# Optimization experiments

Hardware: AMD Instinct MI355X
Metric: run time of the kernel (lower is better)

## Reference

```python
import jax, jax.numpy as jnp
import numpy as np
import math

NUM_BUCKETS = 32
MAX_DISTANCE = 128


def _relative_position_buckets(seq_len):
    # bidirectional T5-style buckets, matching the torch reference exactly
    pos = jnp.arange(seq_len)
    rp = pos[None, :] - pos[:, None]                # [S, S]
    nb = NUM_BUCKETS // 2                            # bidirectional halving
    buckets = (rp > 0).astype(jnp.int32) * nb
    rp = jnp.abs(rp)
    max_exact = nb // 2
    is_small = rp < max_exact
    rp_f = jnp.maximum(rp, 1).astype(jnp.float32)    # avoid log(0); masked by is_small
    rp_large = max_exact + (
        jnp.log(rp_f / max_exact) / math.log(MAX_DISTANCE / max_exact) * (nb - max_exact)
    ).astype(jnp.int32)                              # trunc toward zero, like .to(torch.long)
    rp_large = jnp.minimum(rp_large, nb - 1)
    return buckets + jnp.where(is_small, rp, rp_large)  # [S, S] int32 in [0, 31]


def setup_inputs() -> dict:
    key = jax.random.key(0)
    kq, kk, kv, km, kb = jax.random.split(key, 5)
    B, H, S, D = 4, 4, 2048, 64
    return {
        "query": jax.random.normal(kq, (B, H, S, D), dtype=jnp.float32),
        "key": jax.random.normal(kk, (B, H, S, D), dtype=jnp.float32),
        "value": jax.random.normal(kv, (B, H, S, D), dtype=jnp.float32),
        "mask": jax.random.randint(km, (B, 1, 1, S), 0, 2, dtype=jnp.int32),
        "bias_table": jax.random.normal(kb, (512, 4), dtype=jnp.float32) * 0.02,
    }


def reference(query, key, value, mask, bias_table):
    B, H, S, D = query.shape
    attn = jnp.einsum("bhqd,bhkd->bhqk", query, key)          # [B,H,S,S]
    rel = _relative_position_buckets(S)                        # [S,S]
    bias = bias_table[rel]                                     # [S,S,H]
    bias = jnp.transpose(bias, (2, 0, 1))[None]                # [1,H,S,S]
    scores = (attn + bias) / math.sqrt(D)                      # bias added pre-scale, as in torch
    scores = jnp.where(mask == 0, jnp.float32(-1e9), scores)
    p_attn = jax.nn.softmax(scores, axis=-1)
    out = jnp.einsum("bhqk,bhkd->bhqd", p_attn, value)
    return out, p_attn
```

## Files before the change

kernel.cpp:

```cpp
#include <hip/hip_runtime.h>
#include <math.h>

typedef __attribute__((ext_vector_type(8))) short short8;
typedef __attribute__((ext_vector_type(4))) float f32x4;
typedef _Float16 f16x8 __attribute__((ext_vector_type(8)));
typedef _Float16 f16x4v __attribute__((ext_vector_type(4)));
typedef unsigned short u16;

#define S_LEN 2048
#define D_HEAD 64
#define C2 0.18033688011112043f

static __device__ __forceinline__ float exp2v(float x) {
    float r; asm("v_exp_f32 %0, %1" : "=v"(r) : "v"(x)); return r;
}

static __device__ __forceinline__ void gl_lds16(const void* g, void* l) {
    __builtin_amdgcn_global_load_lds(
        (const __attribute__((address_space(1))) unsigned int*)g,
        (__attribute__((address_space(3))) unsigned int*)l, 16, 0, 0);
}

__global__ void prep_bias(const float* __restrict__ table, float* __restrict__ bias_d) {
    int idx = blockIdx.x * blockDim.x + threadIdx.x;
    if (idx >= 4096) return;
    int delta = idx - 2047;
    int bpos = (delta > 0) ? 16 : 0;
    int ad = delta < 0 ? -delta : delta;
    int rel;
    if (ad < 8) {
        rel = bpos + ad;
    } else {
        float rp = (float)ad;
        int lg = 8 + (int)(logf(rp / 8.0f) / 2.772588722239781f * 8.0f);
        if (lg > 15) lg = 15;
        rel = bpos + lg;
    }
    #pragma unroll
    for (int h = 0; h < 4; ++h)
        bias_d[h * 4096 + idx] = C2 * table[rel * 4 + h];
}

__global__ void prep_half(const float* __restrict__ src, _Float16* __restrict__ dst) {
    size_t i8 = ((size_t)blockIdx.x * 256 + threadIdx.x) * 8;
    f32x4 a = *(const f32x4*)(src + i8);
    f32x4 b = *(const f32x4*)(src + i8 + 4);
    f16x8 h;
    h[0] = (_Float16)a[0]; h[1] = (_Float16)a[1];
    h[2] = (_Float16)a[2]; h[3] = (_Float16)a[3];
    h[4] = (_Float16)b[0]; h[5] = (_Float16)b[1];
    h[6] = (_Float16)b[2]; h[7] = (_Float16)b[3];
    *(f16x8*)(dst + i8) = h;
}

__global__ void prep_vt(const float* __restrict__ V, _Float16* __restrict__ vt) {
    __shared__ float tile[64][65];
    const int bh = blockIdx.y;
    const int k0 = blockIdx.x * 64;
    const int t = threadIdx.x;
    {
        int r = t >> 2, c0 = (t & 3) * 16;
        const float* src = V + ((size_t)bh * S_LEN + k0 + r) * D_HEAD + c0;
        #pragma unroll
        for (int i = 0; i < 16; i += 4) {
            f32x4 v = *(const f32x4*)(src + i);
            tile[r][c0 + i + 0] = v[0];
            tile[r][c0 + i + 1] = v[1];
            tile[r][c0 + i + 2] = v[2];
            tile[r][c0 + i + 3] = v[3];
        }
    }
    __syncthreads();
    {
        int d = t >> 2, kc = (t & 3) * 16;
        size_t ob = ((size_t)bh * D_HEAD + d) * S_LEN + k0 + kc;
        #pragma unroll
        for (int half = 0; half < 2; ++half) {
            f16x8 hv;
            #pragma unroll
            for (int i = 0; i < 8; ++i)
                hv[i] = (_Float16)tile[kc + half * 8 + i][d];
            *(f16x8*)(vt + ob + half * 8) = hv;
        }
    }
}

__launch_bounds__(512, 6)
__global__ void attn_main(const float* __restrict__ Q, const int* __restrict__ mask,
                          const float* __restrict__ bias2,
                          const _Float16* __restrict__ kh_g,
                          const _Float16* __restrict__ vt_g,
                          float* __restrict__ outp, float* __restrict__ p_out) {
    __shared__ __align__(16) char smem[50688];
    _Float16* pbuf = (_Float16*)(smem + 32768);
    float* stats = (float*)(smem + 50176);

    const int tid = threadIdx.x;
    const int w = tid >> 6, l = tid & 63;
    const int wq = w & 3, wk = w >> 2;
    const int g = l >> 4, lq = l & 15;
    const int r7 = lq & 7;
    const int bid = blockIdx.x;
    const int bh = bid & 15, b = bh >> 2, h = bh & 3;
    const int q0 = (bid >> 4) * 64;

    const float* Qp = Q + (size_t)bh * (S_LEN * D_HEAD);
    const int* mp = mask + b * S_LEN;
    const _Float16* khp = kh_g + (size_t)bh * (S_LEN * D_HEAD);
    const _Float16* vhp = vt_g + (size_t)bh * (S_LEN * D_HEAD);

    _Float16* qarea = (_Float16*)smem;
    {
        int sr = tid >> 3, tb = tid & 7;
        const float* src = Qp + (size_t)(q0 + sr) * D_HEAD + tb * 8;
        f32x4 a = *(const f32x4*)src;
        f32x4 c = *(const f32x4*)(src + 4);
        f16x8 hv;
        hv[0] = (_Float16)a[0]; hv[1] = (_Float16)a[1];
        hv[2] = (_Float16)a[2]; hv[3] = (_Float16)a[3];
        hv[4] = (_Float16)c[0]; hv[5] = (_Float16)c[1];
        hv[6] = (_Float16)c[2]; hv[7] = (_Float16)c[3];
        *(f16x8*)(qarea + sr * 64 + ((tb ^ (sr & 7)) * 8)) = hv;
    }
    __syncthreads();
    f16x8 qf[2];
    const int qrow = 16 * wq + lq;
    #pragma unroll
    for (int c = 0; c < 2; ++c)
        qf[c] = *(const f16x8*)(qarea + qrow * 64 + ((4 * c + g) ^ r7) * 8);
    __syncthreads();

    const int qq = q0 + qrow;

    const int rr3 = tid >> 3;
    const int ub0 = (((tid & 7) ^ (rr3 & 7)) * 8);
    const _Float16* s1a = khp + (size_t)rr3 * 64 + ub0;
    gl_lds16(s1a, smem + tid * 16);
    gl_lds16(s1a + 4096, smem + 8192 + tid * 16);
    __syncthreads();

    const int* mP1 = mp + 64 * wk + 4 * g;
    const float* bP1 = bias2 + h * 4096 + 2047 - qq + 64 * wk + 4 * g;
    float lsum = 0.0f;
    for (int t = 0; t < 16; ++t) {
        const char* kb = smem + (t & 1) * 16384;
        int4 mv[4]; float bv[4][4];
        #pragma unroll
        for (int t2 = 0; t2 < 4; ++t2) {
            mv[t2] = *(const int4*)(mP1 + 16 * t2);
            #pragma unroll
            for (int j = 0; j < 4; ++j) bv[t2][j] = bP1[16 * t2 + j];
        }
        if (t < 15) {
            s1a += 8192;
            char* nb = smem + ((t + 1) & 1) * 16384 + tid * 16;
            gl_lds16(s1a, nb);
            gl_lds16(s1a + 4096, nb + 8192);
        }
        __builtin_amdgcn_sched_barrier(0);
        #pragma unroll
        for (int t2 = 0; t2 < 4; ++t2) {
            const int krow = 64 * wk + 16 * t2 + lq;
            f32x4 acc = {0.f, 0.f, 0.f, 0.f};
            #pragma unroll
            for (int c = 0; c < 2; ++c) {
                f16x8 af = *(const f16x8*)(kb + krow * 128 + ((4 * c + g) ^ r7) * 16);
                acc = __builtin_amdgcn_mfma_f32_16x16x32_f16(af, qf[c], acc, 0, 0, 0);
            }
            float s0 = mv[t2].x ? fmaf(acc[0], C2, bv[t2][0]) : -1e9f;
            float s1 = mv[t2].y ? fmaf(acc[1], C2, bv[t2][1]) : -1e9f;
            float s2 = mv[t2].z ? fmaf(acc[2], C2, bv[t2][2]) : -1e9f;
            float s3 = mv[t2].w ? fmaf(acc[3], C2, bv[t2][3]) : -1e9f;
            lsum += exp2v(s0) + exp2v(s1) + exp2v(s2) + exp2v(s3);
        }
        mP1 += 128; bP1 += 128;
        asm volatile("s_waitcnt vmcnt(0)" ::: "memory");
        __builtin_amdgcn_sched_barrier(0);
        __builtin_amdgcn_s_barrier();
        __builtin_amdgcn_sched_barrier(0);
    }
    lsum += __shfl_xor(lsum, 16);
    lsum += __shfl_xor(lsum, 32);
    if (g == 0) stats[wk * 64 + qrow] = lsum;

    const _Float16* sKh = khp + (size_t)rr3 * 64 + ub0;
    const _Float16* sVh = vhp + (size_t)rr3 * 2048 + ub0;
    gl_lds16(sKh, smem + tid * 16);
    gl_lds16(sVh, smem + 8192 + tid * 16);
    __syncthreads();
    float lr2q;
    {
        float L = stats[qrow] + stats[64 + qrow];
        float lg; asm("v_log_f32 %0, %1" : "=v"(lg) : "v"(L));
        lr2q = -lg;
    }

    f32x4 acco[4] = {{0.f,0.f,0.f,0.f},{0.f,0.f,0.f,0.f},{0.f,0.f,0.f,0.f},{0.f,0.f,0.f,0.f}};
    const int* mP = mp + 32 * wk + 4 * g;
    const float* bP = bias2 + h * 4096 + 2047 - qq + 32 * wk + 4 * g;
    const int kAoff0 = (32 * wk + lq) * 128;
    const int voffb = lq * 128 + ((4 * wk + g) ^ r7) * 16;
    _Float16* pwr = pbuf + qrow * 136 + 32 * wk + 4 * g;
    const _Float16* prd = pbuf + qrow * 136 + 32 * wk + 8 * g;
    const int frow = 16 * (w >> 1) + (l >> 4);
    const int fcol = 64 * (w & 1) + (l & 15) * 4;
    const _Float16* frd = pbuf + frow * 136 + fcol;
    float* pF = p_out + (size_t)bh * (S_LEN * S_LEN)
              + (size_t)(q0 + frow) * S_LEN + fcol;

    for (int t = 0; t < 32; ++t) {
        const int cb = (t & 1) * 16384;
        const int pt = (t & 1) * 64;
        int4 mv[2]; float bv[2][4];
        #pragma unroll
        for (int t2 = 0; t2 < 2; ++t2) {
            mv[t2] = *(const int4*)(mP + 16 * t2);
            #pragma unroll
            for (int j = 0; j < 4; ++j) bv[t2][j] = bP[16 * t2 + j];
        }
        if (t < 31) {
            sKh += 4096; sVh += 64;
            char* d0 = smem + ((t + 1) & 1) * 16384 + tid * 16;
            gl_lds16(sKh, d0);
            gl_lds16(sVh, d0 + 8192);
        }
        __builtin_amdgcn_sched_barrier(0);
        #pragma unroll
        for (int t2 = 0; t2 < 2; ++t2) {
            const char* kbase = smem + cb + kAoff0 + t2 * 2048;
            f32x4 acc = {0.f, 0.f, 0.f, 0.f};
            #pragma unroll
            for (int c = 0; c < 2; ++c) {
                f16x8 ah = *(const f16x8*)(kbase + ((4 * c + g) ^ r7) * 16);
                acc = __builtin_amdgcn_mfma_f32_16x16x32_f16(ah, qf[c], acc, 0, 0, 0);
            }
            float p0 = exp2v(mv[t2].x ? fmaf(acc[0], C2, bv[t2][0]) + lr2q : -1e9f);
            float p1 = exp2v(mv[t2].y ? fmaf(acc[1], C2, bv[t2][1]) + lr2q : -1e9f);
            float p2 = exp2v(mv[t2].z ? fmaf(acc[2], C2, bv[t2][2]) + lr2q : -1e9f);
            float p3 = exp2v(mv[t2].w ? fmaf(acc[3], C2, bv[t2][3]) + lr2q : -1e9f);
            f16x4v ph4;
            ph4[0] = (_Float16)p0; ph4[1] = (_Float16)p1;
            ph4[2] = (_Float16)p2; ph4[3] = (_Float16)p3;
            *(f16x4v*)(pwr + pt + 16 * t2) = ph4;
        }
        const f16x8 pf = *(const f16x8*)(prd + pt);
        #pragma unroll
        for (int n = 0; n < 4; ++n) {
            const f16x8 bhf = *(const f16x8*)(smem + cb + 8192 + voffb + n * 2048);
            acco[n] = __builtin_amdgcn_mfma_f32_16x16x32_f16(pf, bhf, acco[n], 0, 0, 0);
        }
        mP += 64; bP += 64;
        if (t & 1) {
            asm volatile("s_waitcnt lgkmcnt(0)" ::: "memory");
            __builtin_amdgcn_sched_barrier(0);
            __builtin_amdgcn_s_barrier();
            __builtin_amdgcn_sched_barrier(0);
            #pragma unroll
            for (int i = 0; i < 4; ++i) {
                f16x4v v = *(const f16x4v*)(frd + i * (4 * 136));
                f32x4 wv;
                wv[0] = (float)v[0]; wv[1] = (float)v[1];
                wv[2] = (float)v[2]; wv[3] = (float)v[3];
                *(f32x4*)(pF + (size_t)(4 * i) * S_LEN) = wv;
            }
            pF += 128;
            __builtin_amdgcn_sched_barrier(0);
            asm volatile("s_waitcnt vmcnt(4)" ::: "memory");
        } else {
            asm volatile("s_waitcnt vmcnt(0)" ::: "memory");
        }
        __builtin_amdgcn_sched_barrier(0);
        __builtin_amdgcn_s_barrier();
        __builtin_amdgcn_sched_barrier(0);
    }

    float* ored = (float*)smem;
    __syncthreads();
    if (wk == 1) {
        #pragma unroll
        for (int n = 0; n < 4; ++n)
            #pragma unroll
            for (int r = 0; r < 4; ++r)
                ored[(wq * 16 + 4 * g + r) * 64 + 16 * n + lq] = acco[n][r];
    }
    __syncthreads();
    if (wk == 0) {
        #pragma unroll
        for (int n = 0; n < 4; ++n) {
            #pragma unroll
            for (int r = 0; r < 4; ++r) {
                float v = acco[n][r] + ored[(wq * 16 + 4 * g + r) * 64 + 16 * n + lq];
                outp[((size_t)bh * S_LEN + q0 + 16 * wq + 4 * g + r) * D_HEAD + 16 * n + lq] = v;
            }
        }
    }
}

extern "C" void kernel_launch(void* const* d_in, const int* in_sizes, int n_in,
                              void* d_out, int out_size, void* d_ws, size_t ws_size,
                              hipStream_t stream) {
    const float* Q = (const float*)d_in[0];
    const float* K = (const float*)d_in[1];
    const float* V = (const float*)d_in[2];
    const int* mask = (const int*)d_in[3];
    const float* table = (const float*)d_in[4];

    float* outp = (float*)d_out;
    float* p_out = outp + (size_t)4 * 4 * 2048 * 64;

    float* bias_d = (float*)d_ws;
    _Float16* kh = (_Float16*)((char*)d_ws + 65536);
    _Float16* vt = kh + (size_t)16 * S_LEN * D_HEAD;

    prep_bias<<<16, 256, 0, stream>>>(table, bias_d);
    prep_half<<<1024, 256, 0, stream>>>(K, kh);
    prep_vt<<<dim3(32, 16), 256, 0, stream>>>(V, vt);
    attn_main<<<512, 512, 0, stream>>>(Q, mask, bias_d, kh, vt, outp, p_out);
}
```

Measured before the change: 104.5 us.

## Switch attention kernel to 4 waves each owning full key range per query block

The main kernel drops from 8 waves (split across query and key halves) to 4 waves, each owning 16 query rows across all keys. This removes the cross-wave LDS reduction of row sums and output accumulators, and gives each wave a private P buffer so the probability stream-out needs no extra block barrier. Mask and bias are premerged, with the log-sum added before the loop. Each thread now issues more MFMAs and global-to-LDS loads per tile, and there are fewer waves per block to hide latency.

```diff
diff --git a/kernel.cpp b/kernel.cpp
--- a/kernel.cpp
+++ b/kernel.cpp
@@ -1,11 +1,9 @@
 #include <hip/hip_runtime.h>
 #include <math.h>
 
-typedef __attribute__((ext_vector_type(8))) short short8;
 typedef __attribute__((ext_vector_type(4))) float f32x4;
 typedef _Float16 f16x8 __attribute__((ext_vector_type(8)));
 typedef _Float16 f16x4v __attribute__((ext_vector_type(4)));
-typedef unsigned short u16;
 
 #define S_LEN 2048
 #define D_HEAD 64
@@ -85,19 +83,16 @@
     }
 }
 
-__launch_bounds__(512, 6)
+__launch_bounds__(256, 3)
 __global__ void attn_main(const float* __restrict__ Q, const int* __restrict__ mask,
                           const float* __restrict__ bias2,
                           const _Float16* __restrict__ kh_g,
                           const _Float16* __restrict__ vt_g,
                           float* __restrict__ outp, float* __restrict__ p_out) {
-    __shared__ __align__(16) char smem[50688];
-    _Float16* pbuf = (_Float16*)(smem + 32768);
-    float* stats = (float*)(smem + 50176);
+    __shared__ __align__(16) char smem[49664];
 
     const int tid = threadIdx.x;
     const int w = tid >> 6, l = tid & 63;
-    const int wq = w & 3, wk = w >> 2;
     const int g = l >> 4, lq = l & 15;
     const int r7 = lq & 7;
     const int bid = blockIdx.x;
@@ -109,69 +104,80 @@
     const _Float16* khp = kh_g + (size_t)bh * (S_LEN * D_HEAD);
     const _Float16* vhp = vt_g + (size_t)bh * (S_LEN * D_HEAD);
 
-    _Float16* qarea = (_Float16*)smem;
+    _Float16* qarea = (_Float16*)(smem + 32768);
     {
-        int sr = tid >> 3, tb = tid & 7;
-        const float* src = Qp + (size_t)(q0 + sr) * D_HEAD + tb * 8;
+        int sr = tid >> 2, tb = tid & 3;
+        const float* src = Qp + (size_t)(q0 + sr) * D_HEAD + tb * 16;
         f32x4 a = *(const f32x4*)src;
         f32x4 c = *(const f32x4*)(src + 4);
-        f16x8 hv;
-        hv[0] = (_Float16)a[0]; hv[1] = (_Float16)a[1];
-        hv[2] = (_Float16)a[2]; hv[3] = (_Float16)a[3];
-        hv[4] = (_Float16)c[0]; hv[5] = (_Float16)c[1];
-        hv[6] = (_Float16)c[2]; hv[7] = (_Float16)c[3];
-        *(f16x8*)(qarea + sr * 64 + ((tb ^ (sr & 7)) * 8)) = hv;
-    }
-    __syncthreads();
-    f16x8 qf[2];
-    const int qrow = 16 * wq + lq;
-    #pragma unroll
-    for (int c = 0; c < 2; ++c)
-        qf[c] = *(const f16x8*)(qarea + qrow * 64 + ((4 * c + g) ^ r7) * 8);
-    __syncthreads();
-
-    const int qq = q0 + qrow;
+        f32x4 d2 = *(const f32x4*)(src + 8);
+        f32x4 e = *(const f32x4*)(src + 12);
+        f16x8 hv0, hv1;
+        hv0[0] = (_Float16)a[0]; hv0[1] = (_Float16)a[1];
+        hv0[2] = (_Float16)a[2]; hv0[3] = (_Float16)a[3];
+        hv0[4] = (_Float16)c[0]; hv0[5] = (_Float16)c[1];
+        hv0[6] = (_Float16)c[2]; hv0[7] = (_Float16)c[3];
+        hv1[0] = (_Float16)d2[0]; hv1[1] = (_Float16)d2[1];
+        hv1[2] = (_Float16)d2[2]; hv1[3] = (_Float16)d2[3];
+        hv1[4] = (_Float16)e[0]; hv1[5] = (_Float16)e[1];
+        hv1[6] = (_Float16)e[2]; hv1[7] = (_Float16)e[3];
+        *(f16x8*)(qarea + sr * 64 + (((2 * tb + 0) ^ (sr & 7)) * 8)) = hv0;
+        *(f16x8*)(qarea + sr * 64 + (((2 * tb + 1) ^ (sr & 7)) * 8)) = hv1;
+    }
 
     const int rr3 = tid >> 3;
     const int ub0 = (((tid & 7) ^ (rr3 & 7)) * 8);
-    const _Float16* s1a = khp + (size_t)rr3 * 64 + ub0;
-    gl_lds16(s1a, smem + tid * 16);
-    gl_lds16(s1a + 4096, smem + 8192 + tid * 16);
-    __syncthreads();
-
-    const int* mP1 = mp + 64 * wk + 4 * g;
-    const float* bP1 = bias2 + h * 4096 + 2047 - qq + 64 * wk + 4 * g;
+    const _Float16* s1 = khp + (size_t)rr3 * 64 + ub0;
+    gl_lds16(s1, smem + tid * 16);
+    gl_lds16(s1 + 2048, smem + 4096 + tid * 16);
+    gl_lds16(s1 + 4096, smem + 8192 + tid * 16);
+    gl_lds16(s1 + 6144, smem + 12288 + tid * 16);
+
+    f16x8 qf[2];
+    const int qrow = 16 * w + lq;
+    qf[0] = *(const f16x8*)(qarea + qrow * 64 + ((g ^ r7) * 8));
+    qf[1] = *(const f16x8*)(qarea + qrow * 64 + (((4 + g) ^ r7) * 8));
+    const int qq = q0 + qrow;
+
+    asm volatile("s_waitcnt vmcnt(0)" ::: "memory");
+    __builtin_amdgcn_s_barrier();
+
+    const int* mP1 = mp + 4 * g;
+    const float* bP1 = bias2 + h * 4096 + 2047 - qq + 4 * g;
     float lsum = 0.0f;
     for (int t = 0; t < 16; ++t) {
         const char* kb = smem + (t & 1) * 16384;
-        int4 mv[4]; float bv[4][4];
-        #pragma unroll
-        for (int t2 = 0; t2 < 4; ++t2) {
-            mv[t2] = *(const int4*)(mP1 + 16 * t2);
-            #pragma unroll
-            for (int j = 0; j < 4; ++j) bv[t2][j] = bP1[16 * t2 + j];
+        f32x4 bvm[8];
+        #pragma unroll
+        for (int t2 = 0; t2 < 8; ++t2) {
+            const int4 mv = *(const int4*)(mP1 + 16 * t2);
+            const f32x4 bv = *(const f32x4*)(bP1 + 16 * t2);
+            bvm[t2][0] = mv.x ? bv[0] : -1e9f;
+            bvm[t2][1] = mv.y ? bv[1] : -1e9f;
+            bvm[t2][2] = mv.z ? bv[2] : -1e9f;
+            bvm[t2][3] = mv.w ? bv[3] : -1e9f;
         }
         if (t < 15) {
-            s1a += 8192;
+            s1 += 8192;
             char* nb = smem + ((t + 1) & 1) * 16384 + tid * 16;
-            gl_lds16(s1a, nb);
-            gl_lds16(s1a + 4096, nb + 8192);
-        }
-        __builtin_amdgcn_sched_barrier(0);
-        #pragma unroll
-        for (int t2 = 0; t2 < 4; ++t2) {
-            const int krow = 64 * wk + 16 * t2 + lq;
+            gl_lds16(s1, nb);
+            gl_lds16(s1 + 2048, nb + 4096);
+            gl_lds16(s1 + 4096, nb + 8192);
+            gl_lds16(s1 + 6144, nb + 12288);
+        }
+        __builtin_amdgcn_sched_barrier(0);
+        #pragma unroll
+        for (int t2 = 0; t2 < 8; ++t2) {
+            const char* base = kb + (16 * t2 + lq) * 128;
+            f16x8 a0 = *(const f16x8*)(base + (g ^ r7) * 16);
+            f16x8 a1 = *(const f16x8*)(base + ((4 + g) ^ r7) * 16);
             f32x4 acc = {0.f, 0.f, 0.f, 0.f};
-            #pragma unroll
-            for (int c = 0; c < 2; ++c) {
-                f16x8 af = *(const f16x8*)(kb + krow * 128 + ((4 * c + g) ^ r7) * 16);
-                acc = __builtin_amdgcn_mfma_f32_16x16x32_f16(af, qf[c], acc, 0, 0, 0);
-            }
-            float s0 = mv[t2].x ? fmaf(acc[0], C2, bv[t2][0]) : -1e9f;
-            float s1 = mv[t2].y ? fmaf(acc[1], C2, bv[t2][1]) : -1e9f;
-            float s2 = mv[t2].z ? fmaf(acc[2], C2, bv[t2][2]) : -1e9f;
-            float s3 = mv[t2].w ? fmaf(acc[3], C2, bv[t2][3]) : -1e9f;
-            lsum += exp2v(s0) + exp2v(s1) + exp2v(s2) + exp2v(s3);
+            acc = __builtin_amdgcn_mfma_f32_16x16x32_f16(a0, qf[0], acc, 0, 0, 0);
+            acc = __builtin_amdgcn_mfma_f32_16x16x32_f16(a1, qf[1], acc, 0, 0, 0);
+            lsum += exp2v(fmaf(acc[0], C2, bvm[t2][0]))
+                  + exp2v(fmaf(acc[1], C2, bvm[t2][1]))
+                  + exp2v(fmaf(acc[2], C2, bvm[t2][2]))
+                  + exp2v(fmaf(acc[3], C2, bvm[t2][3]));
         }
         mP1 += 128; bP1 += 128;
         asm volatile("s_waitcnt vmcnt(0)" ::: "memory");
@@ -181,117 +187,100 @@
     }
     lsum += __shfl_xor(lsum, 16);
     lsum += __shfl_xor(lsum, 32);
-    if (g == 0) stats[wk * 64 + qrow] = lsum;
+    float lr2q;
+    { float lg; asm("v_log_f32 %0, %1" : "=v"(lg) : "v"(lsum)); lr2q = -lg; }
 
     const _Float16* sKh = khp + (size_t)rr3 * 64 + ub0;
     const _Float16* sVh = vhp + (size_t)rr3 * 2048 + ub0;
     gl_lds16(sKh, smem + tid * 16);
+    gl_lds16(sKh + 2048, smem + 4096 + tid * 16);
     gl_lds16(sVh, smem + 8192 + tid * 16);
-    __syncthreads();
-    float lr2q;
-    {
-        float L = stats[qrow] + stats[64 + qrow];
-        float lg; asm("v_log_f32 %0, %1" : "=v"(lg) : "v"(L));
-        lr2q = -lg;
-    }
+    gl_lds16(sVh + 65536, smem + 12288 + tid * 16);
+    asm volatile("s_waitcnt vmcnt(0)" ::: "memory");
+    __builtin_amdgcn_s_barrier();
 
     f32x4 acco[4] = {{0.f,0.f,0.f,0.f},{0.f,0.f,0.f,0.f},{0.f,0.f,0.f,0.f},{0.f,0.f,0.f,0.f}};
-    const int* mP = mp + 32 * wk + 4 * g;
-    const float* bP = bias2 + h * 4096 + 2047 - qq + 32 * wk + 4 * g;
-    const int kAoff0 = (32 * wk + lq) * 128;
-    const int voffb = lq * 128 + ((4 * wk + g) ^ r7) * 16;
-    _Float16* pwr = pbuf + qrow * 136 + 32 * wk + 4 * g;
-    const _Float16* prd = pbuf + qrow * 136 + 32 * wk + 8 * g;
-    const int frow = 16 * (w >> 1) + (l >> 4);
-    const int fcol = 64 * (w & 1) + (l & 15) * 4;
-    const _Float16* frd = pbuf + frow * 136 + fcol;
+    _Float16* pbase = (_Float16*)(smem + 40960) + w * 1088;
+    _Float16* pwr = pbase + lq * 68 + 4 * g;
+    const _Float16* prd = pbase + lq * 68 + 8 * g;
+    const _Float16* frd = pbase + (l >> 4) * 68 + (l & 15) * 4;
     float* pF = p_out + (size_t)bh * (S_LEN * S_LEN)
-              + (size_t)(q0 + frow) * S_LEN + fcol;
+              + (size_t)(q0 + 16 * w + (l >> 4)) * S_LEN + (l & 15) * 4;
+    const int* mPc = mp + 4 * g;
+    const float* bPc = bias2 + h * 4096 + 2047 - qq + 4 * g;
+    const int kAoff = lq * 128;
 
     for (int t = 0; t < 32; ++t) {
         const int cb = (t & 1) * 16384;
-        const int pt = (t & 1) * 64;
-        int4 mv[2]; float bv[2][4];
-        #pragma unroll
-        for (int t2 = 0; t2 < 2; ++t2) {
-            mv[t2] = *(const int4*)(mP + 16 * t2);
-            #pragma unroll
-            for (int j = 0; j < 4; ++j) bv[t2][j] = bP[16 * t2 + j];
+        f32x4 bvm[4];
+        #pragma unroll
+        for (int t2 = 0; t2 < 4; ++t2) {
+            const int4 mv = *(const int4*)(mPc + 16 * t2);
+            const f32x4 bv = *(const f32x4*)(bPc + 16 * t2);
+            bvm[t2][0] = (mv.x ? bv[0] : -1e9f) + lr2q;
+            bvm[t2][1] = (mv.y ? bv[1] : -1e9f) + lr2q;
+            bvm[t2][2] = (mv.z ? bv[2] : -1e9f) + lr2q;
+            bvm[t2][3] = (mv.w ? bv[3] : -1e9f) + lr2q;
         }
         if (t < 31) {
             sKh += 4096; sVh += 64;
-            char* d0 = smem + ((t + 1) & 1) * 16384 + tid * 16;
-            gl_lds16(sKh, d0);
-            gl_lds16(sVh, d0 + 8192);
-        }
-        __builtin_amdgcn_sched_barrier(0);
-        #pragma unroll
-        for (int t2 = 0; t2 < 2; ++t2) {
-            const char* kbase = smem + cb + kAoff0 + t2 * 2048;
+            char* nb = smem + ((t + 1) & 1) * 16384;
+            gl_lds16(sKh, nb + tid * 16);
+            gl_lds16(sKh + 2048, nb + 4096 + tid * 16);
+            gl_lds16(sVh, nb + 8192 + tid * 16);
+            gl_lds16(sVh + 65536, nb + 12288 + tid * 16);
+        }
+        __builtin_amdgcn_sched_barrier(0);
+        #pragma unroll
+        for (int t2 = 0; t2 < 4; ++t2) {
+            const char* base = smem + cb + kAoff + t2 * 2048;
+            f16x8 a0 = *(const f16x8*)(base + (g ^ r7) * 16);
+            f16x8 a1 = *(const f16x8*)(base + ((4 + g) ^ r7) * 16);
             f32x4 acc = {0.f, 0.f, 0.f, 0.f};
-            #pragma unroll
-            for (int c = 0; c < 2; ++c) {
-                f16x8 ah = *(const f16x8*)(kbase + ((4 * c + g) ^ r7) * 16);
-                acc = __builtin_amdgcn_mfma_f32_16x16x32_f16(ah, qf[c], acc, 0, 0, 0);
-            }
-            float p0 = exp2v(mv[t2].x ? fmaf(acc[0], C2, bv[t2][0]) + lr2q : -1e9f);
-            float p1 = exp2v(mv[t2].y ? fmaf(acc[1], C2, bv[t2][1]) + lr2q : -1e9f);
-            float p2 = exp2v(mv[t2].z ? fmaf(acc[2], C2, bv[t2][2]) + lr2q : -1e9f);
-            float p3 = exp2v(mv[t2].w ? fmaf(acc[3], C2, bv[t2][3]) + lr2q : -1e9f);
-            f16x4v ph4;
-            ph4[0] = (_Float16)p0; ph4[1] = (_Float16)p1;
-            ph4[2] = (_Float16)p2; ph4[3] = (_Float16)p3;
-            *(f16x4v*)(pwr + pt + 16 * t2) = ph4;
-        }
-        const f16x8 pf = *(const f16x8*)(prd + pt);
+            acc = __builtin_amdgcn_mfma_f32_16x16x32_f16(a0, qf[0], acc, 0, 0, 0);
+            acc = __builtin_amdgcn_mfma_f32_16x16x32_f16(a1, qf[1], acc, 0, 0, 0);
+            float p0 = exp2v(fmaf(acc[0], C2, bvm[t2][0]));
+            float p1 = exp2v(fmaf(acc[1], C2, bvm[t2][1]));
+            float p2 = exp2v(fmaf(acc[2], C2, bvm[t2][2]));
+            float p3 = exp2v(fmaf(acc[3], C2, bvm[t2][3]));
+            f16x4v ph;
+            ph[0] = (_Float16)p0; ph[1] = (_Float16)p1;
+            ph[2] = (_Float16)p2; ph[3] = (_Float16)p3;
+            *(f16x4v*)(pwr + 16 * t2) = ph;
+        }
+        asm volatile("s_waitcnt lgkmcnt(0)" ::: "memory");
+        __builtin_amdgcn_sched_barrier(0);
+        #pragma unroll
+        for (int i = 0; i < 4; ++i) {
+            f16x4v v = *(const f16x4v*)(frd + i * 272);
+            f32x4 wv;
+            wv[0] = (float)v[0]; wv[1] = (float)v[1];
+            wv[2] = (float)v[2]; wv[3] = (float)v[3];
+            *(f32x4*)(pF + (size_t)(4 * i) * S_LEN) = wv;
+        }
+        const f16x8 pf0 = *(const f16x8*)prd;
+        const f16x8 pf1 = *(const f16x8*)(prd + 32);
         #pragma unroll
         for (int n = 0; n < 4; ++n) {
-            const f16x8 bhf = *(const f16x8*)(smem + cb + 8192 + voffb + n * 2048);
-            acco[n] = __builtin_amdgcn_mfma_f32_16x16x32_f16(pf, bhf, acco[n], 0, 0, 0);
-        }
-        mP += 64; bP += 64;
-        if (t & 1) {
-            asm volatile("s_waitcnt lgkmcnt(0)" ::: "memory");
-            __builtin_amdgcn_sched_barrier(0);
-            __builtin_amdgcn_s_barrier();
-            __builtin_amdgcn_sched_barrier(0);
-            #pragma unroll
-            for (int i = 0; i < 4; ++i) {
-                f16x4v v = *(const f16x4v*)(frd + i * (4 * 136));
-                f32x4 wv;
-                wv[0] = (float)v[0]; wv[1] = (float)v[1];
-                wv[2] = (float)v[2]; wv[3] = (float)v[3];
-                *(f32x4*)(pF + (size_t)(4 * i) * S_LEN) = wv;
-            }
-            pF += 128;
-            __builtin_amdgcn_sched_barrier(0);
-            asm volatile("s_waitcnt vmcnt(4)" ::: "memory");
-        } else {
-            asm volatile("s_waitcnt vmcnt(0)" ::: "memory");
-        }
+            const char* vb = smem + cb + 8192 + lq * 128 + n * 2048;
+            f16x8 b0 = *(const f16x8*)(vb + (g ^ r7) * 16);
+            f16x8 b1 = *(const f16x8*)(vb + ((4 + g) ^ r7) * 16);
+            acco[n] = __builtin_amdgcn_mfma_f32_16x16x32_f16(pf0, b0, acco[n], 0, 0, 0);
+            acco[n] = __builtin_amdgcn_mfma_f32_16x16x32_f16(pf1, b1, acco[n], 0, 0, 0);
+        }
+        mPc += 64; bPc += 64; pF += 64;
+        asm volatile("s_waitcnt vmcnt(4)" ::: "memory");
         __builtin_amdgcn_sched_barrier(0);
         __builtin_amdgcn_s_barrier();
         __builtin_amdgcn_sched_barrier(0);
     }
 
-    float* ored = (float*)smem;
-    __syncthreads();
-    if (wk == 1) {
-        #pragma unroll
-        for (int n = 0; n < 4; ++n)
-            #pragma unroll
-            for (int r = 0; r < 4; ++r)
-                ored[(wq * 16 + 4 * g + r) * 64 + 16 * n + lq] = acco[n][r];
-    }
-    __syncthreads();
-    if (wk == 0) {
-        #pragma unroll
-        for (int n = 0; n < 4; ++n) {
-            #pragma unroll
-            for (int r = 0; r < 4; ++r) {
-                float v = acco[n][r] + ored[(wq * 16 + 4 * g + r) * 64 + 16 * n + lq];
-                outp[((size_t)bh * S_LEN + q0 + 16 * wq + 4 * g + r) * D_HEAD + 16 * n + lq] = v;
-            }
+    #pragma unroll
+    for (int n = 0; n < 4; ++n) {
+        #pragma unroll
+        for (int r = 0; r < 4; ++r) {
+            outp[((size_t)bh * S_LEN + q0 + 16 * w + 4 * g + r) * D_HEAD + 16 * n + lq]
+                = acco[n][r];
         }
     }
 }
@@ -315,5 +304,5 @@
     prep_bias<<<16, 256, 0, stream>>>(table, bias_d);
     prep_half<<<1024, 256, 0, stream>>>(K, kh);
     prep_vt<<<dim3(32, 16), 256, 0, stream>>>(V, vt);
-    attn_main<<<512, 512, 0, stream>>>(Q, mask, bias_d, kh, vt, outp, p_out);
-}
+    attn_main<<<512, 256, 0, stream>>>(Q, mask, bias_d, kh, vt, outp, p_out);
+}
```

New measurement: 114.1 us. 1.09x slower.

## Alternate wave groups between compute and P-store per tile in attention pass

Applied to the files above, without the earlier changes.

Restructures the second attention pass so that the two wave groups (wk) take turns. On each tile one group computes the full 64-key QK^T, exp and PV MFMAs, while the other group writes the previous tile's probabilities from per-wave LDS buffers to global memory and prefetches the next mask/bias, folding the mask and the log-sum term into a bias vector. It also vectorizes the bias loads in the first pass and lowers the occupancy hint in launch_bounds from 6 to 4. The aim is to overlap the large p_attn global store with MFMA work and remove per-iteration mask selects. In exchange, only half the waves do math at any time, and register pressure rises.

```diff
diff --git a/kernel.cpp b/kernel.cpp
--- a/kernel.cpp
+++ b/kernel.cpp
@@ -1,11 +1,9 @@
 #include <hip/hip_runtime.h>
 #include <math.h>
 
-typedef __attribute__((ext_vector_type(8))) short short8;
 typedef __attribute__((ext_vector_type(4))) float f32x4;
 typedef _Float16 f16x8 __attribute__((ext_vector_type(8)));
 typedef _Float16 f16x4v __attribute__((ext_vector_type(4)));
-typedef unsigned short u16;
 
 #define S_LEN 2048
 #define D_HEAD 64
@@ -85,15 +83,14 @@
     }
 }
 
-__launch_bounds__(512, 6)
+__launch_bounds__(512, 4)
 __global__ void attn_main(const float* __restrict__ Q, const int* __restrict__ mask,
                           const float* __restrict__ bias2,
                           const _Float16* __restrict__ kh_g,
                           const _Float16* __restrict__ vt_g,
                           float* __restrict__ outp, float* __restrict__ p_out) {
-    __shared__ __align__(16) char smem[50688];
-    _Float16* pbuf = (_Float16*)(smem + 32768);
-    float* stats = (float*)(smem + 50176);
+    __shared__ __align__(16) char smem[51712];
+    float* stats = (float*)(smem + 51200);
 
     const int tid = threadIdx.x;
     const int w = tid >> 6, l = tid & 63;
@@ -144,12 +141,11 @@
     float lsum = 0.0f;
     for (int t = 0; t < 16; ++t) {
         const char* kb = smem + (t & 1) * 16384;
-        int4 mv[4]; float bv[4][4];
+        int4 mv[4]; f32x4 bv[4];
         #pragma unroll
         for (int t2 = 0; t2 < 4; ++t2) {
             mv[t2] = *(const int4*)(mP1 + 16 * t2);
-            #pragma unroll
-            for (int j = 0; j < 4; ++j) bv[t2][j] = bP1[16 * t2 + j];
+            bv[t2] = *(const f32x4*)(bP1 + 16 * t2);
         }
         if (t < 15) {
             s1a += 8192;
@@ -196,82 +192,105 @@
     }
 
     f32x4 acco[4] = {{0.f,0.f,0.f,0.f},{0.f,0.f,0.f,0.f},{0.f,0.f,0.f,0.f},{0.f,0.f,0.f,0.f}};
-    const int* mP = mp + 32 * wk + 4 * g;
-    const float* bP = bias2 + h * 4096 + 2047 - qq + 32 * wk + 4 * g;
-    const int kAoff0 = (32 * wk + lq) * 128;
-    const int voffb = lq * 128 + ((4 * wk + g) ^ r7) * 16;
-    _Float16* pwr = pbuf + qrow * 136 + 32 * wk + 4 * g;
-    const _Float16* prd = pbuf + qrow * 136 + 32 * wk + 8 * g;
-    const int frow = 16 * (w >> 1) + (l >> 4);
-    const int fcol = 64 * (w & 1) + (l & 15) * 4;
-    const _Float16* frd = pbuf + frow * 136 + fcol;
+    _Float16* pbase = (_Float16*)(smem + 32768) + w * 1152;
+    _Float16* pwr = pbase + lq * 72 + 4 * g;
+    const _Float16* prd = pbase + lq * 72 + 8 * g;
+    const _Float16* frd = pbase + (l >> 4) * 72 + (l & 15) * 4;
     float* pF = p_out + (size_t)bh * (S_LEN * S_LEN)
-              + (size_t)(q0 + frow) * S_LEN + fcol;
+              + (size_t)(q0 + 16 * wq + (l >> 4)) * S_LEN + (l & 15) * 4
+              + 64 * wk;
+    const int* mPc = mp + 4 * g;
+    const float* bPc = bias2 + h * 4096 + 2047 - qq + 4 * g;
+
+    f32x4 bvmr[4];
+    #pragma unroll
+    for (int t2 = 0; t2 < 4; ++t2) {
+        const int4 mv = *(const int4*)(mPc + 64 * wk + 16 * t2);
+        const f32x4 bv = *(const f32x4*)(bPc + 64 * wk + 16 * t2);
+        bvmr[t2][0] = (mv.x ? bv[0] : -1e9f) + lr2q;
+        bvmr[t2][1] = (mv.y ? bv[1] : -1e9f) + lr2q;
+        bvmr[t2][2] = (mv.z ? bv[2] : -1e9f) + lr2q;
+        bvmr[t2][3] = (mv.w ? bv[3] : -1e9f) + lr2q;
+    }
 
     for (int t = 0; t < 32; ++t) {
         const int cb = (t & 1) * 16384;
-        const int pt = (t & 1) * 64;
-        int4 mv[2]; float bv[2][4];
-        #pragma unroll
-        for (int t2 = 0; t2 < 2; ++t2) {
-            mv[t2] = *(const int4*)(mP + 16 * t2);
-            #pragma unroll
-            for (int j = 0; j < 4; ++j) bv[t2][j] = bP[16 * t2 + j];
-        }
+        const bool active = (wk == (t & 1));
         if (t < 31) {
             sKh += 4096; sVh += 64;
             char* d0 = smem + ((t + 1) & 1) * 16384 + tid * 16;
             gl_lds16(sKh, d0);
             gl_lds16(sVh, d0 + 8192);
         }
-        __builtin_amdgcn_sched_barrier(0);
-        #pragma unroll
-        for (int t2 = 0; t2 < 2; ++t2) {
-            const char* kbase = smem + cb + kAoff0 + t2 * 2048;
-            f32x4 acc = {0.f, 0.f, 0.f, 0.f};
-            #pragma unroll
-            for (int c = 0; c < 2; ++c) {
-                f16x8 ah = *(const f16x8*)(kbase + ((4 * c + g) ^ r7) * 16);
-                acc = __builtin_amdgcn_mfma_f32_16x16x32_f16(ah, qf[c], acc, 0, 0, 0);
-            }
-            float p0 = exp2v(mv[t2].x ? fmaf(acc[0], C2, bv[t2][0]) + lr2q : -1e9f);
-            float p1 = exp2v(mv[t2].y ? fmaf(acc[1], C2, bv[t2][1]) + lr2q : -1e9f);
-            float p2 = exp2v(mv[t2].z ? fmaf(acc[2], C2, bv[t2][2]) + lr2q : -1e9f);
-            float p3 = exp2v(mv[t2].w ? fmaf(acc[3], C2, bv[t2][3]) + lr2q : -1e9f);
-            f16x4v ph4;
-            ph4[0] = (_Float16)p0; ph4[1] = (_Float16)p1;
-            ph4[2] = (_Float16)p2; ph4[3] = (_Float16)p3;
-            *(f16x4v*)(pwr + pt + 16 * t2) = ph4;
-        }
-        const f16x8 pf = *(const f16x8*)(prd + pt);
-        #pragma unroll
-        for (int n = 0; n < 4; ++n) {
-            const f16x8 bhf = *(const f16x8*)(smem + cb + 8192 + voffb + n * 2048);
-            acco[n] = __builtin_amdgcn_mfma_f32_16x16x32_f16(pf, bhf, acco[n], 0, 0, 0);
-        }
-        mP += 64; bP += 64;
-        if (t & 1) {
-            asm volatile("s_waitcnt lgkmcnt(0)" ::: "memory");
+        if (active) {
             __builtin_amdgcn_sched_barrier(0);
-            __builtin_amdgcn_s_barrier();
-            __builtin_amdgcn_sched_barrier(0);
-            #pragma unroll
-            for (int i = 0; i < 4; ++i) {
-                f16x4v v = *(const f16x4v*)(frd + i * (4 * 136));
-                f32x4 wv;
-                wv[0] = (float)v[0]; wv[1] = (float)v[1];
-                wv[2] = (float)v[2]; wv[3] = (float)v[3];
-                *(f32x4*)(pF + (size_t)(4 * i) * S_LEN) = wv;
-            }
-            pF += 128;
-            __builtin_amdgcn_sched_barrier(0);
-            asm volatile("s_waitcnt vmcnt(4)" ::: "memory");
+            #pragma unroll
+            for (int t2 = 0; t2 < 4; ++t2) {
+                const char* kbase = smem + cb + (16 * t2 + lq) * 128;
+                f16x8 a0 = *(const f16x8*)(kbase + (g ^ r7) * 16);
+                f16x8 a1 = *(const f16x8*)(kbase + ((4 + g) ^ r7) * 16);
+                f32x4 acc = {0.f, 0.f, 0.f, 0.f};
+                acc = __builtin_amdgcn_mfma_f32_16x16x32_f16(a0, qf[0], acc, 0, 0, 0);
+                acc = __builtin_amdgcn_mfma_f32_16x16x32_f16(a1, qf[1], acc, 0, 0, 0);
+                float p0 = exp2v(fmaf(acc[0], C2, bvmr[t2][0]));
+                float p1 = exp2v(fmaf(acc[1], C2, bvmr[t2][1]));
+                float p2 = exp2v(fmaf(acc[2], C2, bvmr[t2][2]));
+                float p3 = exp2v(fmaf(acc[3], C2, bvmr[t2][3]));
+                f16x4v ph;
+                ph[0] = (_Float16)p0; ph[1] = (_Float16)p1;
+                ph[2] = (_Float16)p2; ph[3] = (_Float16)p3;
+                *(f16x4v*)(pwr + 16 * t2) = ph;
+            }
+            const f16x8 pf0 = *(const f16x8*)prd;
+            const f16x8 pf1 = *(const f16x8*)(prd + 32);
+            #pragma unroll
+            for (int n = 0; n < 4; ++n) {
+                const char* vb = smem + cb + 8192 + (16 * n + lq) * 128;
+                f16x8 b0 = *(const f16x8*)(vb + (g ^ r7) * 16);
+                f16x8 b1 = *(const f16x8*)(vb + ((4 + g) ^ r7) * 16);
+                acco[n] = __builtin_amdgcn_mfma_f32_16x16x32_f16(pf0, b0, acco[n], 0, 0, 0);
+                acco[n] = __builtin_amdgcn_mfma_f32_16x16x32_f16(pf1, b1, acco[n], 0, 0, 0);
+            }
+            asm volatile("s_waitcnt vmcnt(0)" ::: "memory");
         } else {
-            asm volatile("s_waitcnt vmcnt(0)" ::: "memory");
+            if (t > 0) {
+                #pragma unroll
+                for (int i = 0; i < 4; ++i) {
+                    f16x4v v = *(const f16x4v*)(frd + i * 288);
+                    f32x4 wv;
+                    wv[0] = (float)v[0]; wv[1] = (float)v[1];
+                    wv[2] = (float)v[2]; wv[3] = (float)v[3];
+                    *(f32x4*)(pF + (size_t)(4 * i) * S_LEN) = wv;
+                }
+                pF += 128;
+            }
+            if (t < 31) {
+                #pragma unroll
+                for (int t2 = 0; t2 < 4; ++t2) {
+                    const int4 mv = *(const int4*)(mPc + 64 * (t + 1) + 16 * t2);
+                    const f32x4 bv = *(const f32x4*)(bPc + 64 * (t + 1) + 16 * t2);
+                    bvmr[t2][0] = (mv.x ? bv[0] : -1e9f) + lr2q;
+                    bvmr[t2][1] = (mv.y ? bv[1] : -1e9f) + lr2q;
+                    bvmr[t2][2] = (mv.z ? bv[2] : -1e9f) + lr2q;
+                    bvmr[t2][3] = (mv.w ? bv[3] : -1e9f) + lr2q;
+                }
+            }
+            if (t == 0) { asm volatile("s_waitcnt vmcnt(8)" ::: "memory"); }
+            else        { asm volatile("s_waitcnt vmcnt(12)" ::: "memory"); }
         }
         __builtin_amdgcn_sched_barrier(0);
         __builtin_amdgcn_s_barrier();
         __builtin_amdgcn_sched_barrier(0);
+    }
+    if (wk == 1) {
+        #pragma unroll
+        for (int i = 0; i < 4; ++i) {
+            f16x4v v = *(const f16x4v*)(frd + i * 288);
+            f32x4 wv;
+            wv[0] = (float)v[0]; wv[1] = (float)v[1];
+            wv[2] = (float)v[2]; wv[3] = (float)v[3];
+            *(f32x4*)(pF + (size_t)(4 * i) * S_LEN) = wv;
+        }
     }
 
     float* ored = (float*)smem;
```

Measured after the change: 98.45 us. 5.8% less time.
